# Performance work log

Hardware: AMD Instinct MI355X
Metric: run time of the kernel (lower is better)

Reference implementation:

```python
import jax, jax.numpy as jnp
import numpy as np

PARALLEL = 4
EPS = 1e-5

# Binarization with sign (straight-through estimator in bwd; fwd is just sign)
@jax.custom_vjp
def binarize(x):
    return jnp.sign(x)

def _bin_fwd(x):
    return jnp.sign(x), x

def _bin_bwd(x, g):
    return (g * (jnp.abs(x) <= 1.0).astype(g.dtype),)

binarize.defvjp(_bin_fwd, _bin_bwd)


def bconv3x3(x, w, groups, stride=1):
    # XNOR-style conv: binarize activations and weights, grouped 3x3, pad 1
    return jax.lax.conv_general_dilated(
        binarize(x), binarize(w),
        window_strides=(stride, stride),
        padding=[(1, 1), (1, 1)],
        feature_group_count=groups,
        dimension_numbers=('NCHW', 'OIHW', 'NCHW'))


def batchnorm(x, scale, bias, mean, var):
    inv = scale * jax.lax.rsqrt(var + EPS)
    return x * inv[None, :, None, None] + (bias - mean * inv)[None, :, None, None]


def setup_inputs() -> dict:
    key = jax.random.key(0)
    ks = jax.random.split(key, 12)
    f32 = jnp.float32
    return {
        'x':         jax.random.normal(ks[0], (32, 256, 28, 28), dtype=f32),
        'w1':        jax.random.normal(ks[1], (1024, 256, 3, 3), dtype=f32),
        'bn1_scale': jax.random.uniform(ks[2], (1024,), dtype=f32),
        'bn1_bias':  jax.random.normal(ks[3], (1024,), dtype=f32),
        'bn1_mean':  jax.random.normal(ks[4], (1024,), dtype=f32),
        'bn1_var':   jax.random.uniform(ks[5], (1024,), dtype=f32),
        'w2':        jax.random.normal(ks[6], (1024, 256, 3, 3), dtype=f32),
        'bn2_scale': jax.random.uniform(ks[7], (1024,), dtype=f32),
        'bn2_bias':  jax.random.normal(ks[8], (1024,), dtype=f32),
        'bn2_mean':  jax.random.normal(ks[9], (1024,), dtype=f32),
        'bn2_var':   jax.random.uniform(ks[10], (1024,), dtype=f32),
        'lambdas':   jax.random.uniform(ks[11], (4,), dtype=f32),
    }


def reference(x, w1, bn1_scale, bn1_bias, bn1_mean, bn1_var,
              w2, bn2_scale, bn2_bias, bn2_mean, bn2_var, lambdas):
    identity = x  # downsample is None
    # squeeze: repeat channels parallel times -> [B, 1024, H, W]
    xr = jnp.tile(x, (1, PARALLEL, 1, 1))
    out = bconv3x3(xr, w1, groups=PARALLEL, stride=1)
    out = jax.nn.relu(batchnorm(out, bn1_scale, bn1_bias, bn1_mean, bn1_var))
    out = bconv3x3(out, w2, groups=PARALLEL, stride=1)
    out = batchnorm(out, bn2_scale, bn2_bias, bn2_mean, bn2_var)
    B, C, H, W = out.shape
    planes = C // PARALLEL
    # multiplication: per-group scalar lambda, broadcast over planes within each group
    out = out * jnp.repeat(lambdas, planes)[None, :, None, None]
    # squeeze: sum over parallel groups -> [B, planes, H, W]
    out = out.reshape(B, PARALLEL, planes, H, W).sum(axis=1)
    return jax.nn.relu(out + identity)
```

## Files before the change

kernel.cpp:

```cpp
#include <hip/hip_runtime.h>
#include <cstdint>

#define BN_EPS 1e-5f

typedef unsigned int uint;
typedef int v4i __attribute__((ext_vector_type(4)));
typedef int v16i __attribute__((ext_vector_type(16)));
typedef short v4h __attribute__((ext_vector_type(4)));


#define RSTR 7680
#define TILE4 30720

__global__ __launch_bounds__(256) void kPrep(
    const float* __restrict__ s1, const float* __restrict__ b1,
    const float* __restrict__ m1, const float* __restrict__ v1,
    const float* __restrict__ s2, const float* __restrict__ b2,
    const float* __restrict__ m2, const float* __restrict__ v2,
    const float* __restrict__ lam,
    float* __restrict__ thr1, float* __restrict__ bnA2,
    float* __restrict__ bbSum) {
  int t = blockIdx.x * 256 + threadIdx.x;
  if (t >= 1024) return;
  float inv1 = s1[t] / sqrtf(v1[t] + BN_EPS);
  float bb1 = b1[t] - m1[t] * inv1;
  thr1[t] = -bb1 / inv1;
  float inv2 = s2[t] / sqrtf(v2[t] + BN_EPS);
  bnA2[t] = inv2 * lam[t >> 8];
  if (t < 256) {
    float s = 0.f;
#pragma unroll
    for (int g = 0; g < 4; g++) {
      int i = g * 256 + t;
      float iv = s2[i] / sqrtf(v2[i] + BN_EPS);
      s += (b2[i] - m2[i] * iv) * lam[g];
    }
    bbSum[t] = s;
  }
}

__global__ __launch_bounds__(256) void kQ1(const float* __restrict__ x,
                                           char* __restrict__ A1i) {
  const int tid = threadIdx.x;
  const int lane = tid & 63, cb = tid >> 6;
  const int grp = blockIdx.x;
  const int b = grp / 49, p0 = (grp % 49) * 16;
  __shared__ char t[16][256];
  const float4* src =
      (const float4*)(x + ((size_t)(b * 256 + cb * 64 + lane) * 784 + p0));
  float4 f0 = src[0], f1 = src[1], f2 = src[2], f3 = src[3];
  const int c = cb * 64 + lane;
#define Q(V, J) t[J][c] = ((V) >= 0.f) ? (char)1 : (char)-1;
  Q(f0.x, 0)  Q(f0.y, 1)  Q(f0.z, 2)  Q(f0.w, 3)
  Q(f1.x, 4)  Q(f1.y, 5)  Q(f1.z, 6)  Q(f1.w, 7)
  Q(f2.x, 8)  Q(f2.y, 9)  Q(f2.z, 10) Q(f2.w, 11)
  Q(f3.x, 12) Q(f3.y, 13) Q(f3.z, 14) Q(f3.w, 15)
#undef Q
  __syncthreads();
  const int px = tid >> 4, ch = tid & 15;
  *(v4i*)(A1i + (size_t)(b * 784 + p0 + px) * 256 + ch * 16) =
      *(const v4i*)(&t[px][ch * 16]);
}

__global__ __launch_bounds__(256) void kWf(const float* __restrict__ w,
                                           char* __restrict__ Wf) {
  const int oc = blockIdx.x, ic = threadIdx.x;
  const float* s = w + (size_t)(oc * 256 + ic) * 9;
  const int ocb = oc >> 5;
  const int l = (oc & 31) + ((ic >> 4) & 1) * 32;
  const int kk = ic >> 5, j = ic & 15;
  char* base = Wf + (size_t)(ocb * 72 + kk) * 1024 + l * 16 + j;
#pragma unroll
  for (int tap = 0; tap < 9; tap++)
    base[(size_t)tap * 8 * 1024] = (s[tap] >= 0.f) ? (char)1 : (char)-1;
}

__global__ __launch_bounds__(256) void kConv1M(
    const char* __restrict__ A1i, const char* __restrict__ Wf1,
    const float* __restrict__ thr1, char* __restrict__ A2i) {
  const int tid = threadIdx.x;
  const int l = tid & 63, w = tid >> 6;
  const int xg = blockIdx.x;
  const int xcd = xg & 7, s = xg >> 3;
  const int b = xcd * 4 + (s & 3);
  const int rest = s >> 2;
  const int ocq = rest & 3, yt = rest >> 2;
  const int y0 = yt * 2;

  __shared__ char tile[TILE4];
  __shared__ float thrT[256];

  for (int i = tid; i < TILE4 / 16; i += 256) ((v4i*)tile)[i] = (v4i){0,0,0,0};
  thrT[tid] = thr1[ocq * 256 + tid];
  __syncthreads();
  {
    const char* src = A1i + (size_t)b * 784 * 256;
    for (int i = tid; i < 1792; i += 256) {
      int r = i / 448, jj = i - r * 448;
      int px = jj >> 4, ch = jj & 15;
      int ry = y0 - 1 + r;
      if (ry >= 0 && ry < 28) {
        v4i v = *(const v4i*)(src + (size_t)(ry * 28 + px) * 256 + ch * 16);
        int cl = px + 1;
        *(v4i*)(tile + r * RSTR + cl * 256 + ((ch * 16) ^ ((cl & 15) << 4))) = v;
      }
    }
  }
  __syncthreads();

  const int col = l & 31, krow = l >> 5;
  int cbase[2], xm[2][3];
#pragma unroll
  for (int nb = 0; nb < 2; nb++) {
    int px = nb * 32 + col;
    int pxc = (px < 56) ? px : 55;
    int yy = pxc / 28, xx = pxc - yy * 28;
    cbase[nb] = yy * RSTR + xx * 256 + krow * 16;
#pragma unroll
    for (int e = 0; e < 3; e++) xm[nb][e] = ((xx + e) & 15) << 4;
  }

  v16i acc[2][2];
#pragma unroll
  for (int na = 0; na < 2; na++)
#pragma unroll
    for (int nb = 0; nb < 2; nb++) acc[na][nb] = (v16i)(0);
  const char* wb = Wf1 + (size_t)(ocq * 8 + w * 2) * 73728 + l * 16;

  for (int d = 0; d < 3; d++) {
#pragma unroll
    for (int e = 0; e < 3; e++) {
      const char* wp = wb + (size_t)(d * 3 + e) * 8192;
#pragma unroll
      for (int kk = 0; kk < 8; kk++) {
        v4i a0 = *(const v4i*)(wp + kk * 1024);
        v4i a1 = *(const v4i*)(wp + 73728 + kk * 1024);
#pragma unroll
        for (int nb = 0; nb < 2; nb++) {
          int baddr = cbase[nb] + d * RSTR + e * 256 + kk * 32;
          v4i bf = *(const v4i*)(tile + (baddr ^ xm[nb][e]));
          acc[0][nb] = __builtin_amdgcn_mfma_i32_32x32x32_i8(a0, bf, acc[0][nb], 0, 0, 0);
          acc[1][nb] = __builtin_amdgcn_mfma_i32_32x32x32_i8(a1, bf, acc[1][nb], 0, 0, 0);
        }
      }
    }
  }

  __syncthreads();
  char* bt = tile;
#pragma unroll
  for (int na = 0; na < 2; na++) {
#pragma unroll
    for (int nb = 0; nb < 2; nb++) {
      int px = nb * 32 + col;
      if (px < 56) {
#pragma unroll
        for (int q = 0; q < 16; q++) {
          int row = (q & 3) + 8 * (q >> 2) + 4 * krow;
          int ocl = w * 64 + na * 32 + row;
          char bit = ((float)acc[na][nb][q] > thrT[ocl]) ? (char)1 : (char)0;
          bt[px * 256 + (ocl ^ ((px & 15) << 4))] = bit;
        }
      }
    }
  }
  __syncthreads();
  {
    char* dst = A2i + (size_t)(b * 784 + y0 * 28) * 1024 + ocq * 256;
    for (int i = tid; i < 896; i += 256) {
      int p2 = i >> 4, ch = i & 15;
      v4i v = *(const v4i*)(bt + p2 * 256 + ((ch * 16) ^ ((p2 & 15) << 4)));
      *(v4i*)(dst + (size_t)p2 * 1024 + ch * 16) = v;
    }
  }
}

__global__ __launch_bounds__(256) void kConv2P(
    const char* __restrict__ A2i, const char* __restrict__ Wf2,
    short* __restrict__ P16, int b0) {
  const int tid = threadIdx.x;
  const int l = tid & 63, w = tid >> 6;
  const int xg = blockIdx.x;
  const int xcd = xg & 7, s = xg >> 3;
  const int g = xcd >> 1;
  const int bl = (s / 14) * 2 + (xcd & 1);
  const int yt = s % 14;
  const int b = b0 + bl;
  const int y0 = yt * 2;

  __shared__ char tile[TILE4];

  for (int i = tid; i < TILE4 / 16; i += 256) ((v4i*)tile)[i] = (v4i){0,0,0,0};
  __syncthreads();
  {
    const char* src = A2i + (size_t)b * 784 * 1024 + g * 256;
    for (int i = tid; i < 1792; i += 256) {
      int r = i / 448, jj = i - r * 448;
      int px = jj >> 4, ch = jj & 15;
      int ry = y0 - 1 + r;
      if (ry >= 0 && ry < 28) {
        v4i v = *(const v4i*)(src + (size_t)(ry * 28 + px) * 1024 + ch * 16);
        int cl = px + 1;
        *(v4i*)(tile + r * RSTR + cl * 256 + ((ch * 16) ^ ((cl & 15) << 4))) = v;
      }
    }
  }
  __syncthreads();

  const int col = l & 31, krow = l >> 5;
  int cbase[2], xm[2][3];
#pragma unroll
  for (int nb = 0; nb < 2; nb++) {
    int px = nb * 32 + col;
    int pxc = (px < 56) ? px : 55;
    int yy = pxc / 28, xx = pxc - yy * 28;
    cbase[nb] = yy * RSTR + xx * 256 + krow * 16;
#pragma unroll
    for (int e = 0; e < 3; e++) xm[nb][e] = ((xx + e) & 15) << 4;
  }

  v16i acc[2][2];
#pragma unroll
  for (int na = 0; na < 2; na++)
#pragma unroll
    for (int nb = 0; nb < 2; nb++) acc[na][nb] = (v16i)(0);
  const char* wb = Wf2 + (size_t)(g * 8 + w * 2) * 73728 + l * 16;

  for (int d = 0; d < 3; d++) {
#pragma unroll
    for (int e = 0; e < 3; e++) {
      const char* wp = wb + (size_t)(d * 3 + e) * 8192;
#pragma unroll
      for (int kk = 0; kk < 8; kk++) {
        v4i a0 = *(const v4i*)(wp + kk * 1024);
        v4i a1 = *(const v4i*)(wp + 73728 + kk * 1024);
#pragma unroll
        for (int nb = 0; nb < 2; nb++) {
          int baddr = cbase[nb] + d * RSTR + e * 256 + kk * 32;
          v4i bf = *(const v4i*)(tile + (baddr ^ xm[nb][e]));
          acc[0][nb] = __builtin_amdgcn_mfma_i32_32x32x32_i8(a0, bf, acc[0][nb], 0, 0, 0);
          acc[1][nb] = __builtin_amdgcn_mfma_i32_32x32x32_i8(a1, bf, acc[1][nb], 0, 0, 0);
        }
      }
    }
  }

  short* base = P16 + ((size_t)(g * 16 + bl) * 784 + y0 * 28) * 256;
#pragma unroll
  for (int na = 0; na < 2; na++) {
#pragma unroll
    for (int nb = 0; nb < 2; nb++) {
      int px = nb * 32 + col;
      if (px < 56) {
        short* pp = base + px * 256 + w * 64 + na * 32 + 4 * krow;
#pragma unroll
        for (int qg = 0; qg < 4; qg++) {
          v4h v = {(short)acc[na][nb][qg * 4 + 0], (short)acc[na][nb][qg * 4 + 1],
                   (short)acc[na][nb][qg * 4 + 2], (short)acc[na][nb][qg * 4 + 3]};
          *(v4h*)(pp + 8 * qg) = v;
        }
      }
    }
  }
}

__global__ __launch_bounds__(256) void kRed(
    const short* __restrict__ P16, const float* __restrict__ bnA2,
    const float* __restrict__ bbSum, const float* __restrict__ xin,
    float* __restrict__ out, int b0) {
  const int tid = threadIdx.x;
  const int y = blockIdx.x, bl = blockIdx.y, b = b0 + bl;

  __shared__ float vals[256 * 29];

  float cf[4];
#pragma unroll
  for (int g = 0; g < 4; g++) cf[g] = bnA2[g * 256 + tid];
  const float bbs = bbSum[tid];
  const short* Pp[4];
#pragma unroll
  for (int g = 0; g < 4; g++)
    Pp[g] = P16 + ((size_t)(g * 16 + bl) * 784 + y * 28) * 256 + tid;

  for (int x = 0; x < 28; x++) {
    float v = bbs;
#pragma unroll
    for (int g = 0; g < 4; g++)
      v += cf[g] * (float)(int)Pp[g][x * 256];
    vals[tid * 29 + x] = v;
  }
  __syncthreads();

#pragma unroll
  for (int k = 0; k < 7; k++) {
    int f = tid + 256 * k;
    int c = f / 7, xq = f - 7 * c;
    size_t base = ((size_t)(b * 256 + c) * 28 + y) * 28 + xq * 4;
    float4 xi = *(const float4*)(xin + base);
    float4 o;
    o.x = fmaxf(vals[c * 29 + xq * 4 + 0] + xi.x, 0.0f);
    o.y = fmaxf(vals[c * 29 + xq * 4 + 1] + xi.y, 0.0f);
    o.z = fmaxf(vals[c * 29 + xq * 4 + 2] + xi.z, 0.0f);
    o.w = fmaxf(vals[c * 29 + xq * 4 + 3] + xi.w, 0.0f);
    *(float4*)(out + base) = o;
  }
}

extern "C" void kernel_launch(void* const* d_in, const int* in_sizes, int n_in,
                              void* d_out, int out_size, void* d_ws, size_t ws_size,
                              hipStream_t stream) {
  const float* x   = (const float*)d_in[0];
  const float* w1  = (const float*)d_in[1];
  const float* s1  = (const float*)d_in[2];
  const float* b1  = (const float*)d_in[3];
  const float* m1  = (const float*)d_in[4];
  const float* v1  = (const float*)d_in[5];
  const float* w2  = (const float*)d_in[6];
  const float* s2  = (const float*)d_in[7];
  const float* b2  = (const float*)d_in[8];
  const float* m2  = (const float*)d_in[9];
  const float* v2  = (const float*)d_in[10];
  const float* lam = (const float*)d_in[11];
  float* out = (float*)d_out;

  char* ws = (char*)d_ws;
  char*  A1i   = ws + 0;
  char*  Wf1   = ws + 6422528;
  char*  Wf2   = ws + 8781824;
  char*  A2i   = ws + 11141120;
  short* P16   = (short*)(ws + 36831232);
  float* thr1  = (float*)(ws + 62521344);
  float* bnA2  = (float*)(ws + 62525440);
  float* bbSum = (float*)(ws + 62529536);

  kPrep<<<4, 256, 0, stream>>>(s1, b1, m1, v1, s2, b2, m2, v2, lam,
                               thr1, bnA2, bbSum);
  kQ1<<<1568, 256, 0, stream>>>(x, A1i);
  kWf<<<1024, 256, 0, stream>>>(w1, Wf1);
  kWf<<<1024, 256, 0, stream>>>(w2, Wf2);
  kConv1M<<<1792, 256, 0, stream>>>(A1i, Wf1, thr1, A2i);
  for (int b0 = 0; b0 < 32; b0 += 16) {
    kConv2P<<<896, 256, 0, stream>>>(A2i, Wf2, P16, b0);
    kRed<<<dim3(28, 16), 256, 0, stream>>>(P16, bnA2, bbSum, x, out, b0);
  }
}
```

Before: 219.0 us.

## Enlarge conv spatial tiles to four rows and pack threshold bits

Both binary conv kernels now compute four output rows per block instead of two. Each wave holds twice as many MFMA accumulators, so every weight fragment loaded from global memory feeds twice as many MFMAs and the share of halo rows in each block drops. The conv1 epilogue compares four accumulators against a float4 of thresholds and writes one packed 32-bit word instead of four byte stores. If the workspace is large enough, conv2 and the reduction run over all 32 images in one pass instead of two batches. The cost is more LDS and more accumulator registers per block, which lowers occupancy, and half as many blocks are launched.

```diff
diff --git a/kernel.cpp b/kernel.cpp
--- a/kernel.cpp
+++ b/kernel.cpp
@@ -10,7 +10,7 @@
 
 
 #define RSTR 7680
-#define TILE4 30720
+#define TILE6 46080
 
 __global__ __launch_bounds__(256) void kPrep(
     const float* __restrict__ s1, const float* __restrict__ b1,
@@ -82,20 +82,20 @@
   const int l = tid & 63, w = tid >> 6;
   const int xg = blockIdx.x;
   const int xcd = xg & 7, s = xg >> 3;
-  const int b = xcd * 4 + (s & 3);
-  const int rest = s >> 2;
-  const int ocq = rest & 3, yt = rest >> 2;
-  const int y0 = yt * 2;
-
-  __shared__ char tile[TILE4];
+  const int ocq = xcd >> 1;
+  const int b = (s / 7) * 2 + (xcd & 1);
+  const int yt = s % 7;
+  const int y0 = yt * 4;
+
+  __shared__ char tile[TILE6];
   __shared__ float thrT[256];
 
-  for (int i = tid; i < TILE4 / 16; i += 256) ((v4i*)tile)[i] = (v4i){0,0,0,0};
+  for (int i = tid; i < TILE6 / 16; i += 256) ((v4i*)tile)[i] = (v4i){0,0,0,0};
   thrT[tid] = thr1[ocq * 256 + tid];
   __syncthreads();
   {
     const char* src = A1i + (size_t)b * 784 * 256;
-    for (int i = tid; i < 1792; i += 256) {
+    for (int i = tid; i < 2688; i += 256) {
       int r = i / 448, jj = i - r * 448;
       int px = jj >> 4, ch = jj & 15;
       int ry = y0 - 1 + r;
@@ -109,22 +109,22 @@
   __syncthreads();
 
   const int col = l & 31, krow = l >> 5;
-  int cbase[2], xm[2][3];
-#pragma unroll
-  for (int nb = 0; nb < 2; nb++) {
+  int cbase[4], xm[4][3];
+#pragma unroll
+  for (int nb = 0; nb < 4; nb++) {
     int px = nb * 32 + col;
-    int pxc = (px < 56) ? px : 55;
+    int pxc = (px < 112) ? px : 111;
     int yy = pxc / 28, xx = pxc - yy * 28;
     cbase[nb] = yy * RSTR + xx * 256 + krow * 16;
 #pragma unroll
     for (int e = 0; e < 3; e++) xm[nb][e] = ((xx + e) & 15) << 4;
   }
 
-  v16i acc[2][2];
+  v16i acc[2][4];
 #pragma unroll
   for (int na = 0; na < 2; na++)
 #pragma unroll
-    for (int nb = 0; nb < 2; nb++) acc[na][nb] = (v16i)(0);
+    for (int nb = 0; nb < 4; nb++) acc[na][nb] = (v16i)(0);
   const char* wb = Wf1 + (size_t)(ocq * 8 + w * 2) * 73728 + l * 16;
 
   for (int d = 0; d < 3; d++) {
@@ -136,7 +136,7 @@
         v4i a0 = *(const v4i*)(wp + kk * 1024);
         v4i a1 = *(const v4i*)(wp + 73728 + kk * 1024);
 #pragma unroll
-        for (int nb = 0; nb < 2; nb++) {
+        for (int nb = 0; nb < 4; nb++) {
           int baddr = cbase[nb] + d * RSTR + e * 256 + kk * 32;
           v4i bf = *(const v4i*)(tile + (baddr ^ xm[nb][e]));
           acc[0][nb] = __builtin_amdgcn_mfma_i32_32x32x32_i8(a0, bf, acc[0][nb], 0, 0, 0);
@@ -151,15 +151,19 @@
 #pragma unroll
   for (int na = 0; na < 2; na++) {
 #pragma unroll
-    for (int nb = 0; nb < 2; nb++) {
+    for (int nb = 0; nb < 4; nb++) {
       int px = nb * 32 + col;
-      if (px < 56) {
-#pragma unroll
-        for (int q = 0; q < 16; q++) {
-          int row = (q & 3) + 8 * (q >> 2) + 4 * krow;
-          int ocl = w * 64 + na * 32 + row;
-          char bit = ((float)acc[na][nb][q] > thrT[ocl]) ? (char)1 : (char)0;
-          bt[px * 256 + (ocl ^ ((px & 15) << 4))] = bit;
+      if (px < 112) {
+#pragma unroll
+        for (int qg = 0; qg < 4; qg++) {
+          int ocb4 = w * 64 + na * 32 + qg * 8 + 4 * krow;
+          float4 th = *(const float4*)&thrT[ocb4];
+          uint word = 0;
+          word |= ((float)acc[na][nb][qg * 4 + 0] > th.x) ? 0x01u : 0u;
+          word |= ((float)acc[na][nb][qg * 4 + 1] > th.y) ? 0x100u : 0u;
+          word |= ((float)acc[na][nb][qg * 4 + 2] > th.z) ? 0x10000u : 0u;
+          word |= ((float)acc[na][nb][qg * 4 + 3] > th.w) ? 0x1000000u : 0u;
+          *(uint*)(bt + px * 256 + (ocb4 ^ ((px & 15) << 4))) = word;
         }
       }
     }
@@ -167,7 +171,7 @@
   __syncthreads();
   {
     char* dst = A2i + (size_t)(b * 784 + y0 * 28) * 1024 + ocq * 256;
-    for (int i = tid; i < 896; i += 256) {
+    for (int i = tid; i < 1792; i += 256) {
       int p2 = i >> 4, ch = i & 15;
       v4i v = *(const v4i*)(bt + p2 * 256 + ((ch * 16) ^ ((p2 & 15) << 4)));
       *(v4i*)(dst + (size_t)p2 * 1024 + ch * 16) = v;
@@ -177,24 +181,24 @@
 
 __global__ __launch_bounds__(256) void kConv2P(
     const char* __restrict__ A2i, const char* __restrict__ Wf2,
-    short* __restrict__ P16, int b0) {
+    short* __restrict__ P16, int b0, int NBc) {
   const int tid = threadIdx.x;
   const int l = tid & 63, w = tid >> 6;
   const int xg = blockIdx.x;
   const int xcd = xg & 7, s = xg >> 3;
   const int g = xcd >> 1;
-  const int bl = (s / 14) * 2 + (xcd & 1);
-  const int yt = s % 14;
+  const int bl = (s / 7) * 2 + (xcd & 1);
+  const int yt = s % 7;
   const int b = b0 + bl;
-  const int y0 = yt * 2;
-
-  __shared__ char tile[TILE4];
-
-  for (int i = tid; i < TILE4 / 16; i += 256) ((v4i*)tile)[i] = (v4i){0,0,0,0};
+  const int y0 = yt * 4;
+
+  __shared__ char tile[TILE6];
+
+  for (int i = tid; i < TILE6 / 16; i += 256) ((v4i*)tile)[i] = (v4i){0,0,0,0};
   __syncthreads();
   {
     const char* src = A2i + (size_t)b * 784 * 1024 + g * 256;
-    for (int i = tid; i < 1792; i += 256) {
+    for (int i = tid; i < 2688; i += 256) {
       int r = i / 448, jj = i - r * 448;
       int px = jj >> 4, ch = jj & 15;
       int ry = y0 - 1 + r;
@@ -208,22 +212,22 @@
   __syncthreads();
 
   const int col = l & 31, krow = l >> 5;
-  int cbase[2], xm[2][3];
-#pragma unroll
-  for (int nb = 0; nb < 2; nb++) {
+  int cbase[4], xm[4][3];
+#pragma unroll
+  for (int nb = 0; nb < 4; nb++) {
     int px = nb * 32 + col;
-    int pxc = (px < 56) ? px : 55;
+    int pxc = (px < 112) ? px : 111;
     int yy = pxc / 28, xx = pxc - yy * 28;
     cbase[nb] = yy * RSTR + xx * 256 + krow * 16;
 #pragma unroll
     for (int e = 0; e < 3; e++) xm[nb][e] = ((xx + e) & 15) << 4;
   }
 
-  v16i acc[2][2];
+  v16i acc[2][4];
 #pragma unroll
   for (int na = 0; na < 2; na++)
 #pragma unroll
-    for (int nb = 0; nb < 2; nb++) acc[na][nb] = (v16i)(0);
+    for (int nb = 0; nb < 4; nb++) acc[na][nb] = (v16i)(0);
   const char* wb = Wf2 + (size_t)(g * 8 + w * 2) * 73728 + l * 16;
 
   for (int d = 0; d < 3; d++) {
@@ -235,7 +239,7 @@
         v4i a0 = *(const v4i*)(wp + kk * 1024);
         v4i a1 = *(const v4i*)(wp + 73728 + kk * 1024);
 #pragma unroll
-        for (int nb = 0; nb < 2; nb++) {
+        for (int nb = 0; nb < 4; nb++) {
           int baddr = cbase[nb] + d * RSTR + e * 256 + kk * 32;
           v4i bf = *(const v4i*)(tile + (baddr ^ xm[nb][e]));
           acc[0][nb] = __builtin_amdgcn_mfma_i32_32x32x32_i8(a0, bf, acc[0][nb], 0, 0, 0);
@@ -245,13 +249,13 @@
     }
   }
 
-  short* base = P16 + ((size_t)(g * 16 + bl) * 784 + y0 * 28) * 256;
+  short* base = P16 + ((size_t)((g * NBc + bl) * 784) + y0 * 28) * 256;
 #pragma unroll
   for (int na = 0; na < 2; na++) {
 #pragma unroll
-    for (int nb = 0; nb < 2; nb++) {
+    for (int nb = 0; nb < 4; nb++) {
       int px = nb * 32 + col;
-      if (px < 56) {
+      if (px < 112) {
         short* pp = base + px * 256 + w * 64 + na * 32 + 4 * krow;
 #pragma unroll
         for (int qg = 0; qg < 4; qg++) {
@@ -267,7 +271,7 @@
 __global__ __launch_bounds__(256) void kRed(
     const short* __restrict__ P16, const float* __restrict__ bnA2,
     const float* __restrict__ bbSum, const float* __restrict__ xin,
-    float* __restrict__ out, int b0) {
+    float* __restrict__ out, int b0, int NBc) {
   const int tid = threadIdx.x;
   const int y = blockIdx.x, bl = blockIdx.y, b = b0 + bl;
 
@@ -280,7 +284,7 @@
   const short* Pp[4];
 #pragma unroll
   for (int g = 0; g < 4; g++)
-    Pp[g] = P16 + ((size_t)(g * 16 + bl) * 784 + y * 28) * 256 + tid;
+    Pp[g] = P16 + ((size_t)((g * NBc + bl) * 784) + y * 28) * 256 + tid;
 
   for (int x = 0; x < 28; x++) {
     float v = bbs;
@@ -328,19 +332,22 @@
   char*  Wf1   = ws + 6422528;
   char*  Wf2   = ws + 8781824;
   char*  A2i   = ws + 11141120;
-  short* P16   = (short*)(ws + 36831232);
-  float* thr1  = (float*)(ws + 62521344);
-  float* bnA2  = (float*)(ws + 62525440);
-  float* bbSum = (float*)(ws + 62529536);
+  float* thr1  = (float*)(ws + 36831232);
+  float* bnA2  = (float*)(ws + 36835328);
+  float* bbSum = (float*)(ws + 36839424);
+  short* P16   = (short*)(ws + 36843520);
+
+  const size_t needFull = 36843520ull + 4ull * 32 * 784 * 256 * 2;
+  const int NBc = (ws_size >= needFull) ? 32 : 16;
 
   kPrep<<<4, 256, 0, stream>>>(s1, b1, m1, v1, s2, b2, m2, v2, lam,
                                thr1, bnA2, bbSum);
   kQ1<<<1568, 256, 0, stream>>>(x, A1i);
   kWf<<<1024, 256, 0, stream>>>(w1, Wf1);
   kWf<<<1024, 256, 0, stream>>>(w2, Wf2);
-  kConv1M<<<1792, 256, 0, stream>>>(A1i, Wf1, thr1, A2i);
-  for (int b0 = 0; b0 < 32; b0 += 16) {
-    kConv2P<<<896, 256, 0, stream>>>(A2i, Wf2, P16, b0);
-    kRed<<<dim3(28, 16), 256, 0, stream>>>(P16, bnA2, bbSum, x, out, b0);
-  }
-}
+  kConv1M<<<896, 256, 0, stream>>>(A1i, Wf1, thr1, A2i);
+  for (int b0 = 0; b0 < 32; b0 += NBc) {
+    kConv2P<<<8 * (NBc / 2) * 7, 256, 0, stream>>>(A2i, Wf2, P16, b0, NBc);
+    kRed<<<dim3(28, NBc), 256, 0, stream>>>(P16, bnA2, bbSum, x, out, b0, NBc);
+  }
+}
```

Measured after the change: 230.8 us. 1.05x slower.
